# Kernel optimization log

Measured on AMD Instinct MI355X. Metric: run time of the kernel, lower is better.

Reference implementation:

```python
import jax, jax.numpy as jnp
import numpy as np

H = W = 1024
CHUNK = 32  # rows per chunk in the column EDT pass (keeps intermediate at 32*H*W floats)


def setup_inputs() -> dict:
    key = jax.random.key(0)
    k1, k2 = jax.random.split(key)
    preds = jax.random.randint(k1, (H, W), 0, 2).astype(jnp.float32)
    targets = jax.random.randint(k2, (H, W), 0, 2).astype(jnp.float32)
    return {"preds": preds, "targets": targets}


def _edges(seg):
    # morphological erosion via 3x3 box conv, threshold at 9 == kernel.numel()
    s = seg[None, None]  # (1,1,H,W)
    kern = jnp.ones((1, 1, 3, 3), seg.dtype)
    conv = jax.lax.conv_general_dilated(s, kern, (1, 1), ((1, 1), (1, 1)))
    eroded = (conv[0, 0] == 9.0).astype(seg.dtype)
    return seg - eroded


def _edt(edges):
    # exact Euclidean distance transform: distance to nearest zero of (1 - edges),
    # i.e. nearest pixel where edges == 1.  Separable exact algorithm:
    #   1) per-row 1D distance to nearest feature (via cummax/cummin scans)
    #   2) per-column lower envelope min_k g2[k,j] + (i-k)^2 (chunked brute force)
    feat = (1.0 - edges) == 0.0
    Hh, Ww = edges.shape
    BIG = jnp.float32(1e6)
    col = jnp.arange(Ww, dtype=jnp.float32)
    left = col - jax.lax.cummax(jnp.where(feat, col, -BIG), axis=1)
    right = jax.lax.cummin(jnp.where(feat, col, BIG), axis=1, reverse=True) - col
    g = jnp.minimum(jnp.minimum(left, right), BIG)  # row-wise 1D distance
    g2 = g * g  # (H,W) squared row distances
    rows = jnp.arange(Hh, dtype=jnp.float32)

    def chunk(ic):  # ic: (CHUNK,) target row indices
        # (CHUNK, H, W): g2[k,j] + (i-k)^2, min over source row k
        d = g2[None, :, :] + (ic[:, None, None] - rows[None, :, None]) ** 2
        return jnp.min(d, axis=1)  # (CHUNK, W)

    D2 = jax.lax.map(chunk, rows.reshape(-1, CHUNK)).reshape(Hh, Ww)
    return jnp.sqrt(D2)


def reference(preds, targets):
    pred_edges = _edges(preds)
    target_edges = _edges(targets)
    # scipy EDT ran on detached CPU copies -> no gradient through the DTs
    pred_dt = jax.lax.stop_gradient(_edt(pred_edges))
    target_dt = jax.lax.stop_gradient(_edt(target_edges))
    pred_err = target_edges * pred_dt
    target_err = pred_edges * target_dt
    loss = (jnp.mean(pred_err) + jnp.mean(target_err)) / 2.0
    return jax.nn.sigmoid(loss)
```

## Files before the change

kernel.cpp:

```cpp
#include <hip/hip_runtime.h>
#include <math.h>


#define HW 1024
#define RMIN_SENT (1 << 30)
#define WIN 8
#define RPB 128
#define KROWS (RPB + 2 * WIN)
#define HS_STRIDE 17

__global__ __launch_bounds__(256)
void k_rows(const float* __restrict__ pred, const float* __restrict__ targ,
            unsigned short* __restrict__ gp, unsigned short* __restrict__ gt,
            unsigned short* __restrict__ epb, unsigned short* __restrict__ etb)
{
    const int t    = threadIdx.x;
    const int lane = t & 63;
    const int wv   = t >> 6;
    const int r    = blockIdx.x * 4 + wv;
    const int m    = blockIdx.y;
    const float* __restrict__ seg = m ? targ : pred;
    unsigned short* __restrict__ gout = m ? gt : gp;
    unsigned short* __restrict__ ebout = m ? etb : epb;

    const int c0 = lane * 16;

    float cs[16], cm[16], cp[16];
    #pragma unroll
    for (int q = 0; q < 4; ++q)
        *(float4*)&cs[q * 4] = *(const float4*)&seg[r * HW + c0 + q * 4];
    #pragma unroll
    for (int q = 0; q < 4; ++q) {
        *(float4*)&cm[q * 4] = make_float4(0.f, 0.f, 0.f, 0.f);
        *(float4*)&cp[q * 4] = make_float4(0.f, 0.f, 0.f, 0.f);
    }
    if (r > 0) {
        #pragma unroll
        for (int q = 0; q < 4; ++q)
            *(float4*)&cm[q * 4] = *(const float4*)&seg[(r - 1) * HW + c0 + q * 4];
    }
    if (r < HW - 1) {
        #pragma unroll
        for (int q = 0; q < 4; ++q)
            *(float4*)&cp[q * 4] = *(const float4*)&seg[(r + 1) * HW + c0 + q * 4];
    }

    unsigned s_bits = 0, va_bits = 0;
    #pragma unroll
    for (int x = 0; x < 16; ++x) {
        const unsigned s  = (cs[x] != 0.f) ? 1u : 0u;
        const unsigned va = (cs[x] != 0.f && cm[x] != 0.f && cp[x] != 0.f) ? 1u : 0u;
        s_bits  |= s  << x;
        va_bits |= va << x;
    }

    const unsigned vprev = __shfl_up(va_bits, 1);
    const unsigned vnext = __shfl_down(va_bits, 1);
    const unsigned lbit = (lane == 0)  ? 0u : ((vprev >> 15) & 1u);
    const unsigned rbit = (lane == 63) ? 0u : (vnext & 1u);

    const unsigned w18 = (va_bits << 1) | lbit | (rbit << 17);
    const unsigned eroded = w18 & (w18 >> 1) & (w18 >> 2);
    const unsigned edge = s_bits & ~eroded & 0xFFFFu;

    ebout[lane * HW + r] = (unsigned short)edge;

    const int lane_last  = edge ? (c0 + 31 - __clz(edge)) : -1;
    const int lane_first = edge ? (c0 + __ffs(edge) - 1)  : RMIN_SENT;

    int Li = lane_last;
    #pragma unroll
    for (int off = 1; off < 64; off <<= 1) {
        const int v = __shfl_up(Li, off);
        if (lane >= off) Li = max(Li, v);
    }
    int Ri = lane_first;
    #pragma unroll
    for (int off = 1; off < 64; off <<= 1) {
        const int v = __shfl_down(Ri, off);
        if (lane + off < 64) Ri = min(Ri, v);
    }
    int carryL = __shfl_up(Li, 1);   if (lane == 0)  carryL = -1;
    int carryR = __shfl_down(Ri, 1); if (lane == 63) carryR = RMIN_SENT;

    unsigned short gv[16];
    #pragma unroll
    for (int x = 0; x < 16; ++x) {
        const unsigned ble = edge & ((2u << x) - 1u);
        const int L = ble ? (c0 + 31 - __clz(ble)) : carryL;
        const unsigned bge = edge >> x;
        const int R = bge ? (c0 + x + __ffs(bge) - 1) : carryR;
        const int j = c0 + x;
        int g;
        if (L < 0 && R >= RMIN_SENT)      g = 65535;
        else if (L < 0)                   g = R - j;
        else if (R >= RMIN_SENT)          g = j - L;
        else                              g = min(j - L, R - j);
        gv[x] = (unsigned short)g;
    }
    unsigned wpk[8];
    #pragma unroll
    for (int k2 = 0; k2 < 8; ++k2)
        wpk[k2] = (unsigned)gv[2 * k2] | ((unsigned)gv[2 * k2 + 1] << 16);
    uint4 st0, st1;
    st0.x = wpk[0]; st0.y = wpk[1]; st0.z = wpk[2]; st0.w = wpk[3];
    st1.x = wpk[4]; st1.y = wpk[5]; st1.z = wpk[6]; st1.w = wpk[7];
    *(uint4*)&gout[r * HW + c0]     = st0;
    *(uint4*)&gout[r * HW + c0 + 8] = st1;
}

__global__ __launch_bounds__(256)
void k_cols(const unsigned short* __restrict__ gp, const unsigned short* __restrict__ gt,
            const unsigned short* __restrict__ epb, const unsigned short* __restrict__ etb,
            float* __restrict__ partial)
{
    const int j0 = blockIdx.x * 16;
    const int i0 = blockIdx.y * RPB;
    const int m  = blockIdx.z;
    const unsigned short* __restrict__ gg = m ? gt : gp;
    const unsigned short* __restrict__ ewb = m ? epb : etb;

    __shared__ float hs[KROWS * HS_STRIDE];
    __shared__ unsigned short esb[RPB];
    __shared__ float wsum[4];

    for (int idx = threadIdx.x; idx < KROWS * 16; idx += 256) {
        const int kk = idx >> 4, jc = idx & 15;
        const int gk = i0 - WIN + kk;
        float v = 1e30f;
        if ((unsigned)gk < (unsigned)HW) {
            const unsigned gu = gg[gk * HW + j0 + jc];
            float gf = (gu == 65535u) ? (1e6f - (float)(j0 + jc)) : (float)gu;
            v = fmaf(gf, gf, (float)(gk * gk));
        }
        hs[kk * HS_STRIDE + jc] = v;
    }
    if (threadIdx.x < RPB)
        esb[threadIdx.x] = ewb[(j0 >> 4) * HW + i0 + threadIdx.x];
    __syncthreads();

    const int jj = threadIdx.x & 15;
    const int iw = threadIdx.x >> 4;
    float lsum = 0.f;

    #pragma unroll
    for (int g = 0; g < 2; ++g) {
        const int ib = i0 + iw * 8 + g * 4;
        const int kkS = iw * 8 + g * 4;
        float b0 = 3e38f, b1 = 3e38f, b2 = 3e38f, b3 = 3e38f;
        float kf = (float)(ib - WIN);
        const float m0 = -2.f * (float)(ib);
        const float m1 = -2.f * (float)(ib + 1);
        const float m2 = -2.f * (float)(ib + 2);
        const float m3 = -2.f * (float)(ib + 3);
        #pragma unroll
        for (int kk = kkS; kk < kkS + 2 * WIN + 4; ++kk) {
            const float hvv = hs[kk * HS_STRIDE + jj];
            b0 = fminf(b0, fmaf(m0, kf, hvv));
            b1 = fminf(b1, fmaf(m1, kf, hvv));
            b2 = fminf(b2, fmaf(m2, kf, hvv));
            b3 = fminf(b3, fmaf(m3, kf, hvv));
            kf += 1.f;
        }
        const int sLo = max(0, ib - WIN);
        const int sHi = min(HW - 1, ib + WIN + 3);
        float bs[4] = {b0, b1, b2, b3};
        #pragma unroll
        for (int w = 0; w < 4; ++w) {
            const int i = ib + w;
            float D2 = (float)(i * i) + bs[w];
            const int dl = i - sLo + 1, dr = sHi + 1 - i;
            const bool need = ((sLo > 0) && (D2 > (float)(dl * dl))) ||
                              ((sHi < HW - 1) && (D2 > (float)(dr * dr)));
            if (need) {
                float bb = 3e38f, k2 = 0.f;
                const float mm = -2.f * (float)i;
                for (int k = 0; k < HW; ++k) {
                    const unsigned gu = gg[k * HW + j0 + jj];
                    const float gf = (gu == 65535u) ? (1e6f - (float)(j0 + jj))
                                                    : (float)gu;
                    bb = fminf(bb, fmaf(mm, k2, fmaf(gf, gf, k2 * k2)));
                    k2 += 1.f;
                }
                D2 = (float)(i * i) + bb;
            }
            const unsigned wbit = (esb[i - i0] >> jj) & 1u;
            lsum += wbit ? sqrtf(D2) : 0.f;
        }
    }

    #pragma unroll
    for (int off = 32; off > 0; off >>= 1) lsum += __shfl_down(lsum, off);
    if ((threadIdx.x & 63) == 0) wsum[threadIdx.x >> 6] = lsum;
    __syncthreads();
    if (threadIdx.x == 0) {
        const int bid = blockIdx.x + 64 * (blockIdx.y + 8 * blockIdx.z);
        partial[bid] = wsum[0] + wsum[1] + wsum[2] + wsum[3];
    }
}

__global__ __launch_bounds__(256)
void k_fin(const float* __restrict__ partial, float* __restrict__ out)
{
    const int t = threadIdx.x;
    float s = partial[t] + partial[t + 256] + partial[t + 512] + partial[t + 768];
    #pragma unroll
    for (int off = 32; off > 0; off >>= 1) s += __shfl_down(s, off);
    __shared__ float w[4];
    if ((t & 63) == 0) w[t >> 6] = s;
    __syncthreads();
    if (t == 0) {
        const float tot = w[0] + w[1] + w[2] + w[3];
        const float loss = tot * (1.f / (2.f * 1024.f * 1024.f));
        out[0] = 1.f / (1.f + expf(-loss));
    }
}

extern "C" void kernel_launch(void* const* d_in, const int* in_sizes, int n_in,
                              void* d_out, int out_size, void* d_ws, size_t ws_size,
                              hipStream_t stream)
{
    const float* preds   = (const float*)d_in[0];
    const float* targets = (const float*)d_in[1];
    float* out = (float*)d_out;

    char* ws = (char*)d_ws;
    unsigned short* gp  = (unsigned short*)ws;
    unsigned short* gt  = gp + HW * HW;
    unsigned short* epb = gt + HW * HW;
    unsigned short* etb = epb + 64 * HW;
    float* partial = (float*)(etb + 64 * HW);

    dim3 gA(HW / 4, 2, 1);
    k_rows<<<gA, 256, 0, stream>>>(preds, targets, gp, gt, epb, etb);

    dim3 gB(HW / 16, HW / RPB, 2);
    k_cols<<<gB, 256, 0, stream>>>(gp, gt, epb, etb, partial);

    k_fin<<<1, 256, 0, stream>>>(partial, out);
}
```

Before: 74.86 us.

## Fuse row-distance pass into column kernel using ballot bitmasks over local window

```diff
diff --git a/kernel.cpp b/kernel.cpp
--- a/kernel.cpp
+++ b/kernel.cpp
@@ -3,144 +3,107 @@
 
 
 #define HW 1024
-#define RMIN_SENT (1 << 30)
 #define WIN 8
 #define RPB 128
 #define KROWS (RPB + 2 * WIN)
 #define HS_STRIDE 17
 
+__device__ inline int edge_at(const float* __restrict__ seg, int k, int j)
+{
+    if ((unsigned)k >= (unsigned)HW || (unsigned)j >= (unsigned)HW) return 0;
+    if (seg[k * HW + j] == 0.f) return 0;
+    bool all9 = true;
+    #pragma unroll
+    for (int dy = -1; dy <= 1; ++dy)
+        #pragma unroll
+        for (int dx = -1; dx <= 1; ++dx) {
+            const int kk = k + dy, jj = j + dx;
+            const float v = ((unsigned)kk < (unsigned)HW && (unsigned)jj < (unsigned)HW)
+                            ? seg[kk * HW + jj] : 0.f;
+            all9 = all9 && (v != 0.f);
+        }
+    return all9 ? 0 : 1;
+}
+
 __global__ __launch_bounds__(256)
-void k_rows(const float* __restrict__ pred, const float* __restrict__ targ,
-            unsigned short* __restrict__ gp, unsigned short* __restrict__ gt,
-            unsigned short* __restrict__ epb, unsigned short* __restrict__ etb)
+void k_main(const float* __restrict__ pred, const float* __restrict__ targ,
+            float* __restrict__ partial)
 {
     const int t    = threadIdx.x;
     const int lane = t & 63;
     const int wv   = t >> 6;
-    const int r    = blockIdx.x * 4 + wv;
-    const int m    = blockIdx.y;
-    const float* __restrict__ seg = m ? targ : pred;
-    unsigned short* __restrict__ gout = m ? gt : gp;
-    unsigned short* __restrict__ ebout = m ? etb : epb;
-
-    const int c0 = lane * 16;
-
-    float cs[16], cm[16], cp[16];
-    #pragma unroll
-    for (int q = 0; q < 4; ++q)
-        *(float4*)&cs[q * 4] = *(const float4*)&seg[r * HW + c0 + q * 4];
-    #pragma unroll
-    for (int q = 0; q < 4; ++q) {
-        *(float4*)&cm[q * 4] = make_float4(0.f, 0.f, 0.f, 0.f);
-        *(float4*)&cp[q * 4] = make_float4(0.f, 0.f, 0.f, 0.f);
-    }
-    if (r > 0) {
-        #pragma unroll
-        for (int q = 0; q < 4; ++q)
-            *(float4*)&cm[q * 4] = *(const float4*)&seg[(r - 1) * HW + c0 + q * 4];
-    }
-    if (r < HW - 1) {
-        #pragma unroll
-        for (int q = 0; q < 4; ++q)
-            *(float4*)&cp[q * 4] = *(const float4*)&seg[(r + 1) * HW + c0 + q * 4];
-    }
-
-    unsigned s_bits = 0, va_bits = 0;
-    #pragma unroll
-    for (int x = 0; x < 16; ++x) {
-        const unsigned s  = (cs[x] != 0.f) ? 1u : 0u;
-        const unsigned va = (cs[x] != 0.f && cm[x] != 0.f && cp[x] != 0.f) ? 1u : 0u;
-        s_bits  |= s  << x;
-        va_bits |= va << x;
-    }
-
-    const unsigned vprev = __shfl_up(va_bits, 1);
-    const unsigned vnext = __shfl_down(va_bits, 1);
-    const unsigned lbit = (lane == 0)  ? 0u : ((vprev >> 15) & 1u);
-    const unsigned rbit = (lane == 63) ? 0u : (vnext & 1u);
-
-    const unsigned w18 = (va_bits << 1) | lbit | (rbit << 17);
-    const unsigned eroded = w18 & (w18 >> 1) & (w18 >> 2);
-    const unsigned edge = s_bits & ~eroded & 0xFFFFu;
-
-    ebout[lane * HW + r] = (unsigned short)edge;
-
-    const int lane_last  = edge ? (c0 + 31 - __clz(edge)) : -1;
-    const int lane_first = edge ? (c0 + __ffs(edge) - 1)  : RMIN_SENT;
-
-    int Li = lane_last;
-    #pragma unroll
-    for (int off = 1; off < 64; off <<= 1) {
-        const int v = __shfl_up(Li, off);
-        if (lane >= off) Li = max(Li, v);
-    }
-    int Ri = lane_first;
-    #pragma unroll
-    for (int off = 1; off < 64; off <<= 1) {
-        const int v = __shfl_down(Ri, off);
-        if (lane + off < 64) Ri = min(Ri, v);
-    }
-    int carryL = __shfl_up(Li, 1);   if (lane == 0)  carryL = -1;
-    int carryR = __shfl_down(Ri, 1); if (lane == 63) carryR = RMIN_SENT;
-
-    unsigned short gv[16];
-    #pragma unroll
-    for (int x = 0; x < 16; ++x) {
-        const unsigned ble = edge & ((2u << x) - 1u);
-        const int L = ble ? (c0 + 31 - __clz(ble)) : carryL;
-        const unsigned bge = edge >> x;
-        const int R = bge ? (c0 + x + __ffs(bge) - 1) : carryR;
-        const int j = c0 + x;
-        int g;
-        if (L < 0 && R >= RMIN_SENT)      g = 65535;
-        else if (L < 0)                   g = R - j;
-        else if (R >= RMIN_SENT)          g = j - L;
-        else                              g = min(j - L, R - j);
-        gv[x] = (unsigned short)g;
-    }
-    unsigned wpk[8];
-    #pragma unroll
-    for (int k2 = 0; k2 < 8; ++k2)
-        wpk[k2] = (unsigned)gv[2 * k2] | ((unsigned)gv[2 * k2 + 1] << 16);
-    uint4 st0, st1;
-    st0.x = wpk[0]; st0.y = wpk[1]; st0.z = wpk[2]; st0.w = wpk[3];
-    st1.x = wpk[4]; st1.y = wpk[5]; st1.z = wpk[6]; st1.w = wpk[7];
-    *(uint4*)&gout[r * HW + c0]     = st0;
-    *(uint4*)&gout[r * HW + c0 + 8] = st1;
-}
-
-__global__ __launch_bounds__(256)
-void k_cols(const unsigned short* __restrict__ gp, const unsigned short* __restrict__ gt,
-            const unsigned short* __restrict__ epb, const unsigned short* __restrict__ etb,
-            float* __restrict__ partial)
-{
     const int j0 = blockIdx.x * 16;
     const int i0 = blockIdx.y * RPB;
-    const int m  = blockIdx.z;
-    const unsigned short* __restrict__ gg = m ? gt : gp;
-    const unsigned short* __restrict__ ewb = m ? epb : etb;
-
+    const int mc = blockIdx.z;
+    const float* __restrict__ segc = mc ? targ : pred;
+    const float* __restrict__ segw = mc ? pred : targ;
+
+    __shared__ unsigned long long s_mc[146];
+    __shared__ unsigned long long s_me[130];
     __shared__ float hs[KROWS * HS_STRIDE];
     __shared__ unsigned short esb[RPB];
     __shared__ float wsum[4];
 
-    for (int idx = threadIdx.x; idx < KROWS * 16; idx += 256) {
-        const int kk = idx >> 4, jc = idx & 15;
-        const int gk = i0 - WIN + kk;
-        float v = 1e30f;
-        if ((unsigned)gk < (unsigned)HW) {
-            const unsigned gu = gg[gk * HW + j0 + jc];
-            float gf = (gu == 65535u) ? (1e6f - (float)(j0 + jc)) : (float)gu;
-            v = fmaf(gf, gf, (float)(gk * gk));
-        }
-        hs[kk * HS_STRIDE + jc] = v;
-    }
-    if (threadIdx.x < RPB)
-        esb[threadIdx.x] = ewb[(j0 >> 4) * HW + i0 + threadIdx.x];
-    __syncthreads();
-
-    const int jj = threadIdx.x & 15;
-    const int iw = threadIdx.x >> 4;
+    const int W0 = j0 - 24;
+    const int colc = W0 + lane;
+    const bool colok = (unsigned)colc < (unsigned)HW;
+
+    for (int ss = wv; ss < 146; ss += 4) {
+        const int rr = i0 - 9 + ss;
+        unsigned long long m = 0ull;
+        if ((unsigned)rr < (unsigned)HW) {
+            const float v = colok ? segc[rr * HW + colc] : 0.f;
+            m = __ballot(v != 0.f);
+        }
+        if (lane == 0) s_mc[ss] = m;
+    }
+    for (int ss = wv; ss < 130; ss += 4) {
+        const int rr = i0 - 1 + ss;
+        unsigned long long m = 0ull;
+        if ((unsigned)rr < (unsigned)HW) {
+            const float v = colok ? segw[rr * HW + colc] : 0.f;
+            m = __ballot(v != 0.f);
+        }
+        if (lane == 0) s_me[ss] = m;
+    }
+    __syncthreads();
+
+    if (t < KROWS) {
+        const int kr = i0 - WIN + t;
+        if ((unsigned)kr < (unsigned)HW) {
+            const unsigned long long sA = s_mc[t], sB = s_mc[t + 1], sC = s_mc[t + 2];
+            const unsigned long long va = sA & sB & sC;
+            const unsigned long long er = va & (va << 1) & (va >> 1);
+            const unsigned long long edge = (sB & ~er) & 0x7FFFFFFFFFFFFFFEull;
+            const float krk = (float)(kr * kr);
+            #pragma unroll
+            for (int jc = 0; jc < 16; ++jc) {
+                const int p = 24 + jc;
+                const unsigned long long mle = edge & ((1ull << (p + 1)) - 1ull);
+                const unsigned long long mge = edge >> p;
+                int g = 1 << 20;
+                if (mle) g = p - (63 - __clzll((long long)mle));
+                if (mge) g = min(g, __ffsll((unsigned long long)mge) - 1);
+                hs[t * HS_STRIDE + jc] = (g < (1 << 20))
+                    ? fmaf((float)g, (float)g, krk) : 1e30f;
+            }
+        } else {
+            #pragma unroll
+            for (int jc = 0; jc < 16; ++jc)
+                hs[t * HS_STRIDE + jc] = 1e30f;
+        }
+    }
+    if (t < RPB) {
+        const unsigned long long sA = s_me[t], sB = s_me[t + 1], sC = s_me[t + 2];
+        const unsigned long long va = sA & sB & sC;
+        const unsigned long long er = va & (va << 1) & (va >> 1);
+        const unsigned long long edge = sB & ~er;
+        esb[t] = (unsigned short)((edge >> 24) & 0xFFFFull);
+    }
+    __syncthreads();
+
+    const int jj = t & 15;
+    const int iw = t >> 4;
     float lsum = 0.f;
 
     #pragma unroll
@@ -170,19 +133,25 @@
             const int i = ib + w;
             float D2 = (float)(i * i) + bs[w];
             const int dl = i - sLo + 1, dr = sHi + 1 - i;
-            const bool need = ((sLo > 0) && (D2 > (float)(dl * dl))) ||
+            const bool need = (D2 > 576.f) ||
+                              ((sLo > 0) && (D2 > (float)(dl * dl))) ||
                               ((sHi < HW - 1) && (D2 > (float)(dr * dr)));
             if (need) {
-                float bb = 3e38f, k2 = 0.f;
-                const float mm = -2.f * (float)i;
+                const int jg = j0 + jj;
+                float bb = 1e6f - (float)jg;
+                bb = bb * bb;
                 for (int k = 0; k < HW; ++k) {
-                    const unsigned gu = gg[k * HW + j0 + jj];
-                    const float gf = (gu == 65535u) ? (1e6f - (float)(j0 + jj))
-                                                    : (float)gu;
-                    bb = fminf(bb, fmaf(mm, k2, fmaf(gf, gf, k2 * k2)));
-                    k2 += 1.f;
+                    const float rowt = (float)((i - k) * (i - k));
+                    if (rowt >= bb) continue;
+                    for (int d = 0; d < HW; ++d) {
+                        const float dd = rowt + (float)(d * d);
+                        if (dd >= bb) break;
+                        if (edge_at(segc, k, jg - d) || edge_at(segc, k, jg + d)) {
+                            bb = dd; break;
+                        }
+                    }
                 }
-                D2 = (float)(i * i) + bb;
+                D2 = bb;
             }
             const unsigned wbit = (esb[i - i0] >> jj) & 1u;
             lsum += wbit ? sqrtf(D2) : 0.f;
@@ -191,9 +160,9 @@
 
     #pragma unroll
     for (int off = 32; off > 0; off >>= 1) lsum += __shfl_down(lsum, off);
-    if ((threadIdx.x & 63) == 0) wsum[threadIdx.x >> 6] = lsum;
-    __syncthreads();
-    if (threadIdx.x == 0) {
+    if ((t & 63) == 0) wsum[t >> 6] = lsum;
+    __syncthreads();
+    if (t == 0) {
         const int bid = blockIdx.x + 64 * (blockIdx.y + 8 * blockIdx.z);
         partial[bid] = wsum[0] + wsum[1] + wsum[2] + wsum[3];
     }
@@ -224,18 +193,10 @@
     const float* targets = (const float*)d_in[1];
     float* out = (float*)d_out;
 
-    char* ws = (char*)d_ws;
-    unsigned short* gp  = (unsigned short*)ws;
-    unsigned short* gt  = gp + HW * HW;
-    unsigned short* epb = gt + HW * HW;
-    unsigned short* etb = epb + 64 * HW;
-    float* partial = (float*)(etb + 64 * HW);
-
-    dim3 gA(HW / 4, 2, 1);
-    k_rows<<<gA, 256, 0, stream>>>(preds, targets, gp, gt, epb, etb);
-
-    dim3 gB(HW / 16, HW / RPB, 2);
-    k_cols<<<gB, 256, 0, stream>>>(gp, gt, epb, etb, partial);
+    float* partial = (float*)d_ws;
+
+    dim3 gM(HW / 16, HW / RPB, 2);
+    k_main<<<gM, 256, 0, stream>>>(preds, targets, partial);
 
     k_fin<<<1, 256, 0, stream>>>(partial, out);
 }
```

Measured after the change: 93.06 us. 24.3% more time.
